# Optimization experiments

Measured on AMD Instinct MI355X. Metric: run time of the kernel, lower is better.

## Reference

```python
import jax, jax.numpy as jnp
import numpy as np

N, D = 8192, 128
NOISEVAR = 1.0

def _softplusinverse(v):
    return np.log(1.0 - np.exp(-v)) + v

def setup_inputs() -> dict:
    key = jax.random.key(0)
    kx, kn = jax.random.split(key)
    x = jax.random.normal(kx, (N, D), dtype=jnp.float32)
    noise = jax.random.normal(kn, (N, D), dtype=jnp.float32)
    phi = jnp.asarray(_softplusinverse(NOISEVAR), dtype=jnp.float32)
    return {"x": x, "phi": phi, "noise": noise}

def reference(x, phi, noise):
    # x: [n, d] encoded features; phi: scalar noise param; noise: [n, d] i.i.d. N(0,1)
    n = x.shape[0]
    var = jax.nn.softplus(phi)
    # Pairwise squared L2 distances via Gram-matrix trick (same math as
    # norm(x_i - x_j)^2, avoids the [n, n, d] broadcast intermediate).
    sq = jnp.sum(x * x, axis=1)                                  # [n]
    d2 = jnp.maximum(sq[:, None] + sq[None, :] - 2.0 * (x @ x.T), 0.0)  # [n, n]
    kde_contribution = jnp.mean(jax.nn.logsumexp(-0.5 * d2 / var, axis=1))
    IXT_nats = jnp.log(jnp.float32(n)) - kde_contribution
    IXT = IXT_nats / jnp.log(jnp.float32(2.0))  # bits=True -> nats2bits
    out = x + var * noise                        # training=True noise injection
    return out, IXT
```

## Files before the change

kernel.cpp:

```cpp
#include <hip/hip_runtime.h>
#include <hip/hip_bf16.h>

#define N 8192
#define D 128
#define T64 64
#define NT64 (N / T64)
#define NPAIR (NT64 * (NT64 + 1) / 2)

typedef __attribute__((ext_vector_type(8))) short short8;
typedef __attribute__((ext_vector_type(4))) float floatx4;
typedef unsigned int u32;

static __device__ inline float softplus_of(const float* __restrict__ phi) {
    float p = phi[0];
    return (p > 20.f) ? p : log1pf(__expf(p));
}

static __device__ inline unsigned short f2bf(float f) {
    return __builtin_bit_cast(unsigned short, __float2bfloat16(f));
}

static __device__ inline short8 pack8(float4 a, float4 b) {
    short8 r;
    r[0] = (short)f2bf(a.x); r[1] = (short)f2bf(a.y);
    r[2] = (short)f2bf(a.z); r[3] = (short)f2bf(a.w);
    r[4] = (short)f2bf(b.x); r[5] = (short)f2bf(b.y);
    r[6] = (short)f2bf(b.z); r[7] = (short)f2bf(b.w);
    return r;
}

__global__ __launch_bounds__(256) void k1_prep(
        const float* __restrict__ x, const float* __restrict__ phi,
        const float* __restrict__ noise, float* __restrict__ out,
        unsigned short* __restrict__ bf16x, float* __restrict__ sq,
        float* __restrict__ rowsum) {
    int gid = blockIdx.x * 256 + threadIdx.x;
    int row = gid >> 4;
    int gc  = gid & 15;
    float var = softplus_of(phi);

    const float* xs = x     + (size_t)row * D + gc * 8;
    const float* ns = noise + (size_t)row * D + gc * 8;
    float4 u  = *(const float4*)xs, v  = *(const float4*)(xs + 4);
    float4 nu = *(const float4*)ns, nv = *(const float4*)(ns + 4);

    float4 o0, o1;
    o0.x = u.x + var * nu.x; o0.y = u.y + var * nu.y;
    o0.z = u.z + var * nu.z; o0.w = u.w + var * nu.w;
    o1.x = v.x + var * nv.x; o1.y = v.y + var * nv.y;
    o1.z = v.z + var * nv.z; o1.w = v.w + var * nv.w;
    float* od = out + (size_t)row * D + gc * 8;
    *(float4*)od = o0; *(float4*)(od + 4) = o1;

    short8 p = pack8(u, v);
    *(short8*)&bf16x[(size_t)row * D + (size_t)(gc ^ (row & 15)) * 8] = p;

    float s = 0.f;
    #pragma unroll
    for (int k = 0; k < 8; k++) {
        u32 bits = ((u32)(unsigned short)p[k]) << 16;
        float b = __builtin_bit_cast(float, bits);
        s += b * b;
    }
    #pragma unroll
    for (int m = 1; m < 16; m <<= 1) s += __shfl_xor(s, m, 64);
    if (gc == 0) { sq[row] = s; rowsum[row] = 0.f; }
}

__global__ __launch_bounds__(256, 2) void k2_gram(
        const unsigned short* __restrict__ bf16x, const float* __restrict__ phi,
        const float* __restrict__ sq, float* __restrict__ rowsum) {
    const int w    = blockIdx.x * 4 + (threadIdx.x >> 6);
    const int lane = threadIdx.x & 63;
    const int lrow = lane & 15;
    const int quad = lane >> 4;

    const int cnt = (w < 64) ? 5 : 4;
    int start     = (w < 64) ? 5 * w : 4 * w + 64;
    int ti = 0, rem = start, len = NT64;
    while (rem >= len) { rem -= len; ++ti; --len; }
    int tj = ti + rem;

    float var = softplus_of(phi);
    const float e2c = (-0.5f / var) * 1.4426950408889634f;
    const float m2c = -2.0f * e2c;

    short8 af[4][4], bf[4][4];
    float  sie[4][4], rowAcc[4][4];
    int curTi = -1;

    {
        const unsigned short* bb = bf16x + (size_t)tj * T64 * D;
        #pragma unroll
        for (int nt = 0; nt < 4; nt++) {
            const unsigned short* br = bb + (size_t)(nt * 16 + lrow) * D;
            #pragma unroll
            for (int kk = 0; kk < 4; kk++)
                bf[nt][kk] = *(const short8*)&br[((kk * 4 + quad) ^ lrow) * 8];
        }
    }

    for (int r = 0; r < cnt; ++r) {
        const int iB = ti * T64, jB = tj * T64;

        float sje[4];
        #pragma unroll
        for (int nt = 0; nt < 4; nt++)
            sje[nt] = sq[jB + nt * 16 + lrow] * e2c;

        if (ti != curTi) {
            if (curTi >= 0) {
                const int pB = curTi * T64;
                #pragma unroll
                for (int mt = 0; mt < 4; mt++)
                    #pragma unroll
                    for (int reg = 0; reg < 4; reg++) {
                        float vv = rowAcc[mt][reg];
                        #pragma unroll
                        for (int m = 1; m < 16; m <<= 1) vv += __shfl_xor(vv, m, 64);
                        if (lrow == 0)
                            atomicAdd(&rowsum[pB + mt * 16 + quad * 4 + reg], vv);
                    }
            }
            #pragma unroll
            for (int mt = 0; mt < 4; mt++) {
                const unsigned short* ar = bf16x + (size_t)(iB + mt * 16 + lrow) * D;
                #pragma unroll
                for (int kk = 0; kk < 4; kk++)
                    af[mt][kk] = *(const short8*)&ar[((kk * 4 + quad) ^ lrow) * 8];
            }
            #pragma unroll
            for (int mt = 0; mt < 4; mt++)
                #pragma unroll
                for (int reg = 0; reg < 4; reg++) {
                    sie[mt][reg] = sq[iB + mt * 16 + quad * 4 + reg] * e2c;
                    rowAcc[mt][reg] = 0.f;
                }
            curTi = ti;
        }

        int nti = ti, ntj = tj + 1;
        if (ntj == NT64) { ++nti; ntj = nti; }

        float colAcc[4] = {0.f, 0.f, 0.f, 0.f};
        #pragma unroll
        for (int nt = 0; nt < 4; nt++) {
            floatx4 acc[4] = {};
            #pragma unroll
            for (int kk = 0; kk < 4; kk++)
                #pragma unroll
                for (int mt = 0; mt < 4; mt++)
                    acc[mt] = __builtin_amdgcn_mfma_f32_16x16x32_bf16(
                        af[mt][kk], bf[nt][kk], acc[mt], 0, 0, 0);

            if (nt == 3 && r + 1 < cnt) {
                const unsigned short* bb = bf16x + (size_t)ntj * T64 * D;
                #pragma unroll
                for (int n2 = 0; n2 < 4; n2++) {
                    const unsigned short* br = bb + (size_t)(n2 * 16 + lrow) * D;
                    #pragma unroll
                    for (int kk = 0; kk < 4; kk++)
                        bf[n2][kk] = *(const short8*)&br[((kk * 4 + quad) ^ lrow) * 8];
                }
            }

            float sj = sje[nt];
            #pragma unroll
            for (int mt = 0; mt < 4; mt++)
                #pragma unroll
                for (int reg = 0; reg < 4; reg++) {
                    float p2 = fminf(fmaf(acc[mt][reg], m2c, sie[mt][reg] + sj), 0.f);
                    float p  = __builtin_amdgcn_exp2f(p2);
                    rowAcc[mt][reg] += p;
                    colAcc[nt]      += p;
                }
        }

        if (ti != tj) {
            #pragma unroll
            for (int nt = 0; nt < 4; nt++) {
                float vv = colAcc[nt];
                vv += __shfl_xor(vv, 16, 64);
                vv += __shfl_xor(vv, 32, 64);
                if (quad == 0)
                    atomicAdd(&rowsum[jB + nt * 16 + lrow], vv);
            }
        }

        ti = nti; tj = ntj;
    }

    {
        const int pB = curTi * T64;
        #pragma unroll
        for (int mt = 0; mt < 4; mt++)
            #pragma unroll
            for (int reg = 0; reg < 4; reg++) {
                float vv = rowAcc[mt][reg];
                #pragma unroll
                for (int m = 1; m < 16; m <<= 1) vv += __shfl_xor(vv, m, 64);
                if (lrow == 0)
                    atomicAdd(&rowsum[pB + mt * 16 + quad * 4 + reg], vv);
            }
    }
}

__global__ __launch_bounds__(1024) void k3_final(
        const float* __restrict__ rowsum, float* __restrict__ out_ixt) {
    __shared__ float red[16];
    int t = threadIdx.x;
    float local = 0.f;
    for (int i = t; i < N; i += 1024) local += logf(rowsum[i]);
    #pragma unroll
    for (int m = 1; m < 64; m <<= 1) local += __shfl_xor(local, m, 64);
    if ((t & 63) == 0) red[t >> 6] = local;
    __syncthreads();
    if (t < 16) {
        float v = red[t];
        #pragma unroll
        for (int m = 1; m < 16; m <<= 1) v += __shfl_xor(v, m, 64);
        if (t == 0) {
            float kde = v / (float)N;
            out_ixt[0] = (logf((float)N) - kde) * 1.4426950408889634f;
        }
    }
}

extern "C" void kernel_launch(void* const* d_in, const int* in_sizes, int n_in,
                              void* d_out, int out_size, void* d_ws, size_t ws_size,
                              hipStream_t stream) {
    const float* x     = (const float*)d_in[0];
    const float* phi   = (const float*)d_in[1];
    const float* noise = (const float*)d_in[2];
    float* out = (float*)d_out;

    float* rowsum = (float*)d_ws;
    float* sq     = rowsum + N;
    unsigned short* bf16x = (unsigned short*)(sq + N);

    k1_prep<<<(N * 16) / 256, 256, 0, stream>>>(x, phi, noise, out, bf16x, sq, rowsum);
    k2_gram<<<512, 256, 0, stream>>>(bf16x, phi, sq, rowsum);
    k3_final<<<1, 1024, 0, stream>>>(rowsum, out + (size_t)N * D);
}
```

Before: 98.62 us.

## Quantize features to int8 and compute Gram matrix with i8 MFMA

After: 101.9 us. 3.3% more time.

```diff
diff --git a/kernel.cpp b/kernel.cpp
--- a/kernel.cpp
+++ b/kernel.cpp
@@ -5,34 +5,19 @@
 #define D 128
 #define T64 64
 #define NT64 (N / T64)
-#define NPAIR (NT64 * (NT64 + 1) / 2)
-
-typedef __attribute__((ext_vector_type(8))) short short8;
-typedef __attribute__((ext_vector_type(4))) float floatx4;
-typedef unsigned int u32;
+
+typedef __attribute__((ext_vector_type(4))) int   intx4;
+typedef unsigned long long u64;
 
 static __device__ inline float softplus_of(const float* __restrict__ phi) {
     float p = phi[0];
     return (p > 20.f) ? p : log1pf(__expf(p));
 }
 
-static __device__ inline unsigned short f2bf(float f) {
-    return __builtin_bit_cast(unsigned short, __float2bfloat16(f));
-}
-
-static __device__ inline short8 pack8(float4 a, float4 b) {
-    short8 r;
-    r[0] = (short)f2bf(a.x); r[1] = (short)f2bf(a.y);
-    r[2] = (short)f2bf(a.z); r[3] = (short)f2bf(a.w);
-    r[4] = (short)f2bf(b.x); r[5] = (short)f2bf(b.y);
-    r[6] = (short)f2bf(b.z); r[7] = (short)f2bf(b.w);
-    return r;
-}
-
 __global__ __launch_bounds__(256) void k1_prep(
         const float* __restrict__ x, const float* __restrict__ phi,
         const float* __restrict__ noise, float* __restrict__ out,
-        unsigned short* __restrict__ bf16x, float* __restrict__ sq,
+        signed char* __restrict__ q8, int* __restrict__ sqv,
         float* __restrict__ rowsum) {
     int gid = blockIdx.x * 256 + threadIdx.x;
     int row = gid >> 4;
@@ -52,61 +37,56 @@
     float* od = out + (size_t)row * D + gc * 8;
     *(float4*)od = o0; *(float4*)(od + 4) = o1;
 
-    short8 p = pack8(u, v);
-    *(short8*)&bf16x[(size_t)row * D + (size_t)(gc ^ (row & 15)) * 8] = p;
-
-    float s = 0.f;
+    float f[8] = {u.x, u.y, u.z, u.w, v.x, v.y, v.z, v.w};
+    u64 pack = 0;
+    int s = 0;
     #pragma unroll
     for (int k = 0; k < 8; k++) {
-        u32 bits = ((u32)(unsigned short)p[k]) << 16;
-        float b = __builtin_bit_cast(float, bits);
-        s += b * b;
-    }
+        float c = fminf(fmaxf(f[k] * 16.f, -127.f), 127.f);
+        int q = (int)rintf(c);
+        s += q * q;
+        pack |= ((u64)(q & 255)) << (8 * k);
+    }
+    *(u64*)&q8[(size_t)row * D + gc * 8] = pack;
+
     #pragma unroll
     for (int m = 1; m < 16; m <<= 1) s += __shfl_xor(s, m, 64);
-    if (gc == 0) { sq[row] = s; rowsum[row] = 0.f; }
-}
-
-__global__ __launch_bounds__(256, 2) void k2_gram(
-        const unsigned short* __restrict__ bf16x, const float* __restrict__ phi,
-        const float* __restrict__ sq, float* __restrict__ rowsum) {
+    if (gc == 0) { sqv[row] = s; rowsum[row] = 0.f; }
+}
+
+__global__ __launch_bounds__(256, 3) void k2_gram(
+        const signed char* __restrict__ q8, const float* __restrict__ phi,
+        const int* __restrict__ sqv, float* __restrict__ rowsum) {
     const int w    = blockIdx.x * 4 + (threadIdx.x >> 6);
     const int lane = threadIdx.x & 63;
     const int lrow = lane & 15;
     const int quad = lane >> 4;
 
-    const int cnt = (w < 64) ? 5 : 4;
-    int start     = (w < 64) ? 5 * w : 4 * w + 64;
+    const int cnt = (w < 2112) ? 3 : 2;
+    int start     = (w < 2112) ? 3 * w : 2 * w + 2112;
     int ti = 0, rem = start, len = NT64;
     while (rem >= len) { rem -= len; ++ti; --len; }
     int tj = ti + rem;
 
     float var = softplus_of(phi);
-    const float e2c = (-0.5f / var) * 1.4426950408889634f;
-    const float m2c = -2.0f * e2c;
-
-    short8 af[4][4], bf[4][4];
-    float  sie[4][4], rowAcc[4][4];
+    const float c2 = ((-0.5f / var) * 1.4426950408889634f) * (1.f / 256.f);
+
+    intx4 af[4][2], bf[4][2];
+    int   sqi[4][4];
+    float rowAcc[4][4];
+    int   sje[4], sjeN[4];
     int curTi = -1;
 
-    {
-        const unsigned short* bb = bf16x + (size_t)tj * T64 * D;
-        #pragma unroll
-        for (int nt = 0; nt < 4; nt++) {
-            const unsigned short* br = bb + (size_t)(nt * 16 + lrow) * D;
-            #pragma unroll
-            for (int kk = 0; kk < 4; kk++)
-                bf[nt][kk] = *(const short8*)&br[((kk * 4 + quad) ^ lrow) * 8];
-        }
+    #pragma unroll
+    for (int nt = 0; nt < 4; nt++) {
+        const signed char* br = q8 + (size_t)(tj * T64 + nt * 16 + lrow) * D + quad * 16;
+        bf[nt][0] = *(const intx4*)br;
+        bf[nt][1] = *(const intx4*)(br + 64);
+        sje[nt] = sqv[tj * T64 + nt * 16 + lrow];
     }
 
     for (int r = 0; r < cnt; ++r) {
         const int iB = ti * T64, jB = tj * T64;
-
-        float sje[4];
-        #pragma unroll
-        for (int nt = 0; nt < 4; nt++)
-            sje[nt] = sq[jB + nt * 16 + lrow] * e2c;
 
         if (ti != curTi) {
             if (curTi >= 0) {
@@ -124,16 +104,16 @@
             }
             #pragma unroll
             for (int mt = 0; mt < 4; mt++) {
-                const unsigned short* ar = bf16x + (size_t)(iB + mt * 16 + lrow) * D;
-                #pragma unroll
-                for (int kk = 0; kk < 4; kk++)
-                    af[mt][kk] = *(const short8*)&ar[((kk * 4 + quad) ^ lrow) * 8];
+                const signed char* ar =
+                    q8 + (size_t)(iB + mt * 16 + lrow) * D + quad * 16;
+                af[mt][0] = *(const intx4*)ar;
+                af[mt][1] = *(const intx4*)(ar + 64);
             }
             #pragma unroll
             for (int mt = 0; mt < 4; mt++)
                 #pragma unroll
                 for (int reg = 0; reg < 4; reg++) {
-                    sie[mt][reg] = sq[iB + mt * 16 + quad * 4 + reg] * e2c;
+                    sqi[mt][reg] = sqv[iB + mt * 16 + quad * 4 + reg];
                     rowAcc[mt][reg] = 0.f;
                 }
             curTi = ti;
@@ -141,36 +121,38 @@
 
         int nti = ti, ntj = tj + 1;
         if (ntj == NT64) { ++nti; ntj = nti; }
+        const bool more = (r + 1 < cnt);
 
         float colAcc[4] = {0.f, 0.f, 0.f, 0.f};
         #pragma unroll
         for (int nt = 0; nt < 4; nt++) {
-            floatx4 acc[4] = {};
-            #pragma unroll
-            for (int kk = 0; kk < 4; kk++)
+            intx4 acc[4] = {};
+            #pragma unroll
+            for (int kk = 0; kk < 2; kk++)
                 #pragma unroll
                 for (int mt = 0; mt < 4; mt++)
-                    acc[mt] = __builtin_amdgcn_mfma_f32_16x16x32_bf16(
+                    acc[mt] = __builtin_amdgcn_mfma_i32_16x16x64_i8(
                         af[mt][kk], bf[nt][kk], acc[mt], 0, 0, 0);
 
-            if (nt == 3 && r + 1 < cnt) {
-                const unsigned short* bb = bf16x + (size_t)ntj * T64 * D;
-                #pragma unroll
-                for (int n2 = 0; n2 < 4; n2++) {
-                    const unsigned short* br = bb + (size_t)(n2 * 16 + lrow) * D;
+            if (more) {
+                const signed char* br =
+                    q8 + (size_t)(ntj * T64 + nt * 16 + lrow) * D + quad * 16;
+                bf[nt][0] = *(const intx4*)br;
+                bf[nt][1] = *(const intx4*)(br + 64);
+                if (nt == 3) {
                     #pragma unroll
-                    for (int kk = 0; kk < 4; kk++)
-                        bf[n2][kk] = *(const short8*)&br[((kk * 4 + quad) ^ lrow) * 8];
+                    for (int n2 = 0; n2 < 4; n2++)
+                        sjeN[n2] = sqv[ntj * T64 + n2 * 16 + lrow];
                 }
             }
 
-            float sj = sje[nt];
+            int sj = sje[nt];
             #pragma unroll
             for (int mt = 0; mt < 4; mt++)
                 #pragma unroll
                 for (int reg = 0; reg < 4; reg++) {
-                    float p2 = fminf(fmaf(acc[mt][reg], m2c, sie[mt][reg] + sj), 0.f);
-                    float p  = __builtin_amdgcn_exp2f(p2);
+                    int d2s = sqi[mt][reg] + sj - 2 * acc[mt][reg];
+                    float p = __builtin_amdgcn_exp2f((float)d2s * c2);
                     rowAcc[mt][reg] += p;
                     colAcc[nt]      += p;
                 }
@@ -187,6 +169,10 @@
             }
         }
 
+        if (more) {
+            #pragma unroll
+            for (int nt = 0; nt < 4; nt++) sje[nt] = sjeN[nt];
+        }
         ti = nti; tj = ntj;
     }
 
@@ -235,10 +221,10 @@
     float* out = (float*)d_out;
 
     float* rowsum = (float*)d_ws;
-    float* sq     = rowsum + N;
-    unsigned short* bf16x = (unsigned short*)(sq + N);
-
-    k1_prep<<<(N * 16) / 256, 256, 0, stream>>>(x, phi, noise, out, bf16x, sq, rowsum);
-    k2_gram<<<512, 256, 0, stream>>>(bf16x, phi, sq, rowsum);
+    int*   sqv    = (int*)(rowsum + N);
+    signed char* q8 = (signed char*)(sqv + N);
+
+    k1_prep<<<(N * 16) / 256, 256, 0, stream>>>(x, phi, noise, out, q8, sqv, rowsum);
+    k2_gram<<<768, 256, 0, stream>>>(q8, phi, sqv, rowsum);
     k3_final<<<1, 1024, 0, stream>>>(rowsum, out + (size_t)N * D);
 }
```
